# Performance work log

Hardware: AMD Instinct MI355X
Metric: run time of the kernel (lower is better)

Reference implementation:

```python
import jax, jax.numpy as jnp
import numpy as np

B, N, D, DS, LAT, FD, NF = 2, 384, 128, 3, 256, 1, 2
NPOS = DS * (2 * 5 + 1)  # 3 + 3*2*5 = 33
FREQS = np.linspace(1.0, 32.0, 5)  # torch.linspace(1, 2**5, 5)
EPS = 1e-5


def _bn(x, g, b):
    # BatchNorm1d, train-mode batch stats: normalize per channel over (batch, points)
    m = jnp.mean(x, axis=(0, 1))
    v = jnp.var(x, axis=(0, 1))
    return (x - m) * jax.lax.rsqrt(v + EPS) * g + b


def _tblock(xyz4, f, Wq, Wk, Wv, Wg1, bg1, Wg2, bg2, Wpe, bpe, g, b):
    # group_all=True full vector attention. f: [B,n,D], xyz4: [B,n,3]
    q = f @ Wq.T
    k = f @ Wk.T
    v = f @ Wv.T
    # knn_xyz gathered under no_grad in torch -> stop_gradient on the key side
    pd = xyz4[:, :, None] - jax.lax.stop_gradient(xyz4)[:, None]  # [B,n,n,3]
    parts = [pd]
    for fr in FREQS:
        parts.append(jnp.sin(pd * fr))
        parts.append(jnp.cos(pd * fr))
    pos = jnp.concatenate(parts, axis=-1) @ Wpe.T + bpe  # [B,n,n,D]
    edges = q[:, :, None] - k[:, None] + pos  # [B,n,n,D]
    h = jax.nn.relu(edges @ Wg1.T + bg1)
    attn = jax.nn.softmax(h @ Wg2.T + bg2, axis=-2)  # softmax over neighbor axis
    res = jnp.sum(attn * (v[:, None] + pos), axis=2)  # einsum bmnf,bmnf->bmf
    return _bn(res + f, g, b)


def setup_inputs() -> dict:
    key = jax.random.key(0)
    ks = iter(jax.random.split(key, 40))
    def rn(shape, s=0.05):
        return jax.random.normal(next(ks), shape, dtype=jnp.float32) * s
    z = lambda *s: jnp.zeros(s, jnp.float32)
    o = lambda *s: jnp.ones(s, jnp.float32)
    nb = NF + 1  # begin block + nfinal blocks
    return {
        "xyz": jax.random.normal(next(ks), (B, N, DS), dtype=jnp.float32),
        "feats": jax.random.normal(next(ks), (B, N, FD), dtype=jnp.float32),
        "enc_W": rn((D, FD)), "enc_b": z(D),
        "tb_Wq": rn((nb, D, D)), "tb_Wk": rn((nb, D, D)), "tb_Wv": rn((nb, D, D)),
        "tb_Wg1": rn((nb, D, D)), "tb_bg1": z(nb, D),
        "tb_Wg2": rn((nb, D, D)), "tb_bg2": z(nb, D),
        "tb_Wpe": rn((nb, D, NPOS)), "tb_bpe": z(nb, D),
        "tb_gamma": o(nb, D), "tb_beta": z(nb, D),
        "em_W1": rn((NF, D, D)), "em_b1": z(NF, D),
        "em_W2": rn((NF, D, D)), "em_b2": z(NF, D),
        "em_gamma": o(NF, D), "em_beta": z(NF, D),
        "fcf_W1": rn((LAT, D)), "fcf_b1": z(LAT),
        "fcf_W2": rn((LAT, LAT)), "fcf_b2": z(LAT),
    }


def reference(xyz, feats, enc_W, enc_b, tb_Wq, tb_Wk, tb_Wv, tb_Wg1, tb_bg1,
              tb_Wg2, tb_bg2, tb_Wpe, tb_bpe, tb_gamma, tb_beta,
              em_W1, em_b1, em_W2, em_b2, em_gamma, em_beta,
              fcf_W1, fcf_b1, fcf_W2, fcf_b2):
    f = feats @ enc_W.T + enc_b  # enc_feats
    x4 = xyz * 4.0
    for i in range(NF + 1):  # i=0: transformer_begin; i>=1: final transformers
        f = _tblock(x4, f, tb_Wq[i], tb_Wk[i], tb_Wv[i], tb_Wg1[i], tb_bg1[i],
                    tb_Wg2[i], tb_bg2[i], tb_Wpe[i], tb_bpe[i], tb_gamma[i], tb_beta[i])
        if i > 0:
            j = i - 1  # ElementwiseMLP: bn(x + relu(conv2(relu(conv1(x)))))
            y = jax.nn.relu(f @ em_W1[j].T + em_b1[j])
            y = jax.nn.relu(y @ em_W2[j].T + em_b2[j])
            f = _bn(f + y, em_gamma[j], em_beta[j])
    e = jax.nn.relu(f @ fcf_W1.T + fcf_b1) @ fcf_W2.T + fcf_b2
    return jnp.max(e, axis=1)  # lat_rep [B, lat_dim]
```

## Files before the change

### kernel.cpp

```cpp
#include <hip/hip_runtime.h>
#include <hip/hip_bf16.h>

#define B_ 2
#define N_ 384
#define D_ 128
#define LAT_ 256
#define NPOS_ 33
#define ROWS_ (B_*N_)

typedef __attribute__((ext_vector_type(8))) short bf16x8;
typedef __attribute__((ext_vector_type(4))) float f32x4;

#define MFMA(a,b,c) __builtin_amdgcn_mfma_f32_16x16x32_bf16((a),(b),(c),0,0,0)

__device__ __forceinline__ unsigned short f2bf(float x) {
    unsigned int u = __float_as_uint(x);
    u += 0x7FFFu + ((u >> 16) & 1u);
    return (unsigned short)(u >> 16);
}

__device__ __forceinline__ float bn_apply(float x, const float* stats, const float* gam,
                                          const float* bet, int d) {
    float s  = stats[d], sq = stats[128 + d];
    float mean = s * (1.f/ROWS_);
    float var  = sq * (1.f/ROWS_) - mean*mean;
    return (x - mean) * rsqrtf(var + 1e-5f) * gam[d] + bet[d];
}

__global__ __launch_bounds__(256) void enc_kernel(const float* __restrict__ feats,
                           const float* __restrict__ W,
                           const float* __restrict__ bias,
                           float* __restrict__ f) {
    int i = blockIdx.x*256 + threadIdx.x;
    if (i >= ROWS_*D_) return;
    int r = i >> 7, d = i & 127;
    f[i] = feats[r]*W[d] + bias[d];
}

__global__ __launch_bounds__(128) void qkv_kernel(const float* __restrict__ graw,
    const float* __restrict__ stats, const float* __restrict__ gam, const float* __restrict__ bet,
    int use_stats,
    const float* __restrict__ Wq, const float* __restrict__ Wk, const float* __restrict__ Wv,
    float* __restrict__ q, float* __restrict__ k, float* __restrict__ v) {
    __shared__ float row[D_];
    int r = blockIdx.x, d = threadIdx.x;
    float x = graw[r*D_+d];
    if (use_stats) x = bn_apply(x, stats, gam, bet, d);
    row[d] = x;
    __syncthreads();
    float aq=0.f, ak=0.f, av=0.f;
    #pragma unroll 4
    for (int e4=0;e4<D_/4;e4++){
        float4 wq = *(const float4*)(Wq + d*D_ + e4*4);
        float4 wk = *(const float4*)(Wk + d*D_ + e4*4);
        float4 wv = *(const float4*)(Wv + d*D_ + e4*4);
        float x0=row[e4*4+0], x1=row[e4*4+1], x2=row[e4*4+2], x3=row[e4*4+3];
        aq += wq.x*x0 + wq.y*x1 + wq.z*x2 + wq.w*x3;
        ak += wk.x*x0 + wk.y*x1 + wk.z*x2 + wk.w*x3;
        av += wv.x*x0 + wv.y*x1 + wv.z*x2 + wv.w*x3;
    }
    q[r*D_+d]=aq; k[r*D_+d]=ak; v[r*D_+d]=av;
}

__global__ __launch_bounds__(512) void attn_mfma_kernel(
    const float* __restrict__ xyz, const float* __restrict__ graw,
    const float* __restrict__ stats_in, const float* __restrict__ gam_in,
    const float* __restrict__ bet_in, int use_stats,
    const float* __restrict__ qb, const float* __restrict__ kb, const float* __restrict__ vb,
    const float* __restrict__ Wpe, const float* __restrict__ bpe,
    const float* __restrict__ Wg1, const float* __restrict__ bg1,
    const float* __restrict__ Wg2, const float* __restrict__ bg2,
    float* __restrict__ gout, float* __restrict__ stats_out)
{
    __shared__ unsigned short sParts[32*64];
    __shared__ unsigned short sX[32*128];
    __shared__ unsigned short sH[32*128];
    __shared__ float sRed[4*128];

    const int t   = threadIdx.x;
    const int w   = t >> 6;
    const int l   = t & 63;
    const int lr  = l & 15;
    const int lg  = l >> 4;
    const int rb  = w >> 2;
    const int ct0 = (w & 3) * 2;

    const int row  = blockIdx.x;
    const int b    = row / N_;
    const int brow = b * N_;

    bf16x8 bWg1[2][4], bWg2[2][4], bWpe[2][2];
    float  bpe_c[2], bg1_c[2], bg2_c[2], q_c[2];

    #pragma unroll
    for (int ct = 0; ct < 2; ++ct) {
        const int dout = (ct0 + ct) * 16 + lr;
        #pragma unroll
        for (int kt = 0; kt < 4; ++kt) {
            const float* p1 = Wg1 + dout * D_ + kt * 32 + lg * 8;
            const float* p2 = Wg2 + dout * D_ + kt * 32 + lg * 8;
            float4 a0 = *(const float4*)(p1);
            float4 a1 = *(const float4*)(p1 + 4);
            float4 c0 = *(const float4*)(p2);
            float4 c1 = *(const float4*)(p2 + 4);
            bf16x8 v1, v2;
            v1[0]=(short)f2bf(a0.x); v1[1]=(short)f2bf(a0.y); v1[2]=(short)f2bf(a0.z); v1[3]=(short)f2bf(a0.w);
            v1[4]=(short)f2bf(a1.x); v1[5]=(short)f2bf(a1.y); v1[6]=(short)f2bf(a1.z); v1[7]=(short)f2bf(a1.w);
            v2[0]=(short)f2bf(c0.x); v2[1]=(short)f2bf(c0.y); v2[2]=(short)f2bf(c0.z); v2[3]=(short)f2bf(c0.w);
            v2[4]=(short)f2bf(c1.x); v2[5]=(short)f2bf(c1.y); v2[6]=(short)f2bf(c1.z); v2[7]=(short)f2bf(c1.w);
            bWg1[ct][kt] = v1;
            bWg2[ct][kt] = v2;
        }
        #pragma unroll
        for (int kt = 0; kt < 2; ++kt) {
            bf16x8 vv;
            #pragma unroll
            for (int e = 0; e < 8; ++e) {
                const int p = kt*32 + lg*8 + e;
                const float x = (p < NPOS_) ? Wpe[dout*NPOS_ + p] : 0.f;
                vv[e] = (short)f2bf(x);
            }
            bWpe[ct][kt] = vv;
        }
        bpe_c[ct] = bpe[dout];
        bg1_c[ct] = bg1[dout];
        bg2_c[ct] = bg2[dout];
        q_c[ct]   = qb[row*D_ + dout];
    }

    const float x4m0 = 4.f*xyz[row*3+0];
    const float x4m1 = 4.f*xyz[row*3+1];
    const float x4m2 = 4.f*xyz[row*3+2];

    for (int i = t; i < 32*64/2; i += 512) ((unsigned int*)sParts)[i] = 0u;
    __syncthreads();

    auto partsgen = [&](int n0) {
        const int n = t >> 4, j = t & 15;
        const int nr = (brow + n0 + n) * 3;
        const float pd0 = x4m0 - 4.f*xyz[nr+0];
        const float pd1 = x4m1 - 4.f*xyz[nr+1];
        const float pd2 = x4m2 - 4.f*xyz[nr+2];
        auto pval = [&](int p) -> float {
            if (p < 3) return p==0?pd0:(p==1?pd1:pd2);
            const int qq = p - 3;
            const int fi = qq / 6;
            int rem = qq - fi*6;
            bool is_sin = true;
            if (rem >= 3) { rem -= 3; is_sin = false; }
            const float pdj = rem==0?pd0:(rem==1?pd1:pd2);
            const float fr = fi==0?1.f:(fi==1?8.75f:(fi==2?16.5f:(fi==3?24.25f:32.f)));
            const float a = pdj * fr;
            return is_sin ? __sinf(a) : __cosf(a);
        };
        const int sw = (n & 7) << 3;
        sParts[(n*64 + j)      ^ sw] = f2bf(pval(j));
        sParts[(n*64 + j + 16) ^ sw] = f2bf(pval(j + 16));
        if (j == 0) sParts[(n*64 + 32) ^ sw] = f2bf(pval(32));
    };

    f32x4 pos[2];
    auto posedges = [&](int n0) {
        #pragma unroll
        for (int ct = 0; ct < 2; ++ct) {
            f32x4 acc = {0.f, 0.f, 0.f, 0.f};
            #pragma unroll
            for (int kt = 0; kt < 2; ++kt) {
                const int r16 = rb*16 + lr;
                const int idx = (r16*64 + kt*32 + lg*8) ^ ((r16 & 7) << 3);
                bf16x8 a = *(const bf16x8*)&sParts[idx];
                acc = MFMA(a, bWpe[ct][kt], acc);
            }
            #pragma unroll
            for (int r = 0; r < 4; ++r) acc[r] += bpe_c[ct];
            pos[ct] = acc;
        }
        #pragma unroll
        for (int ct = 0; ct < 2; ++ct) {
            const int d = (ct0 + ct)*16 + lr;
            #pragma unroll
            for (int r = 0; r < 4; ++r) {
                const int nl = rb*16 + lg*4 + r;
                const float e = pos[ct][r] + q_c[ct] - kb[(brow + n0 + nl)*D_ + d];
                sX[(nl*128 + d) ^ ((nl & 7) << 3)] = f2bf(e);
            }
        }
    };

    partsgen(0);
    __syncthreads();
    posedges(0);
    __syncthreads();

    float res_p[2] = {0.f, 0.f}, s_p[2] = {0.f, 0.f};

    for (int it = 0; it < N_/32; ++it) {
        const int n0 = it * 32;

        f32x4 hacc[2];
        hacc[0] = (f32x4){bg1_c[0], bg1_c[0], bg1_c[0], bg1_c[0]};
        hacc[1] = (f32x4){bg1_c[1], bg1_c[1], bg1_c[1], bg1_c[1]};
        #pragma unroll
        for (int kt = 0; kt < 4; ++kt) {
            const int r16 = rb*16 + lr;
            const int idx = (r16*128 + kt*32 + lg*8) ^ ((r16 & 7) << 3);
            bf16x8 a = *(const bf16x8*)&sX[idx];
            hacc[0] = MFMA(a, bWg1[0][kt], hacc[0]);
            hacc[1] = MFMA(a, bWg1[1][kt], hacc[1]);
        }
        #pragma unroll
        for (int ct = 0; ct < 2; ++ct) {
            const int d = (ct0 + ct)*16 + lr;
            #pragma unroll
            for (int r = 0; r < 4; ++r) {
                const int nl = rb*16 + lg*4 + r;
                sH[(nl*128 + d) ^ ((nl & 7) << 3)] = f2bf(fmaxf(hacc[ct][r], 0.f));
            }
        }
        __syncthreads();

        f32x4 lacc[2];
        lacc[0] = (f32x4){bg2_c[0], bg2_c[0], bg2_c[0], bg2_c[0]};
        lacc[1] = (f32x4){bg2_c[1], bg2_c[1], bg2_c[1], bg2_c[1]};
        #pragma unroll
        for (int kt = 0; kt < 4; ++kt) {
            const int r16 = rb*16 + lr;
            const int idx = (r16*128 + kt*32 + lg*8) ^ ((r16 & 7) << 3);
            bf16x8 a = *(const bf16x8*)&sH[idx];
            lacc[0] = MFMA(a, bWg2[0][kt], lacc[0]);
            lacc[1] = MFMA(a, bWg2[1][kt], lacc[1]);
        }
        #pragma unroll
        for (int ct = 0; ct < 2; ++ct) {
            const int d = (ct0 + ct)*16 + lr;
            #pragma unroll
            for (int r = 0; r < 4; ++r) {
                const int nl = rb*16 + lg*4 + r;
                const float wgt = __expf(lacc[ct][r]);
                const float vp = vb[(brow + n0 + nl)*D_ + d] + pos[ct][r];
                res_p[ct] += wgt * vp;
                s_p[ct]   += wgt;
            }
        }
        if (it < N_/32 - 1) partsgen(n0 + 32);
        __syncthreads();

        if (it < N_/32 - 1) {
            posedges(n0 + 32);
            __syncthreads();
        }
    }

    #pragma unroll
    for (int ct = 0; ct < 2; ++ct) {
        #pragma unroll
        for (int off = 16; off < 64; off <<= 1) {
            res_p[ct] += __shfl_xor(res_p[ct], off, 64);
            s_p[ct]   += __shfl_xor(s_p[ct], off, 64);
        }
    }
    if (lg < 2) {
        const int d = (ct0 + lg)*16 + lr;
        sRed[(rb*2+0)*128 + d] = (lg == 0) ? res_p[0] : res_p[1];
        sRed[(rb*2+1)*128 + d] = (lg == 0) ? s_p[0]   : s_p[1];
    }
    __syncthreads();
    if (t < D_) {
        const float rsum = sRed[t]       + sRed[2*128 + t];
        const float ssum = sRed[128 + t] + sRed[3*128 + t];
        float fres = graw[row*D_ + t];
        if (use_stats) fres = bn_apply(fres, stats_in, gam_in, bet_in, t);
        const float val = rsum / ssum + fres;
        gout[row*D_ + t] = val;
        atomicAdd(&stats_out[t], val);
        atomicAdd(&stats_out[128 + t], val*val);
    }
}

__global__ __launch_bounds__(128) void em_kernel(const float* __restrict__ graw,
    const float* __restrict__ stats_in, const float* __restrict__ gam_in, const float* __restrict__ bet_in,
    const float* __restrict__ W1, const float* __restrict__ b1,
    const float* __restrict__ W2, const float* __restrict__ b2,
    float* __restrict__ gout, float* __restrict__ stats_out)
{
    __shared__ float row[D_], y1[D_];
    int r = blockIdx.x, d = threadIdx.x;
    float fn = bn_apply(graw[r*D_+d], stats_in, gam_in, bet_in, d);
    row[d] = fn; __syncthreads();
    float a = b1[d];
    #pragma unroll 4
    for (int e4=0;e4<D_/4;e4++){
        float4 w = *(const float4*)(W1 + d*D_ + e4*4);
        a += w.x*row[e4*4+0] + w.y*row[e4*4+1] + w.z*row[e4*4+2] + w.w*row[e4*4+3];
    }
    y1[d] = fmaxf(a,0.f); __syncthreads();
    float a2 = b2[d];
    #pragma unroll 4
    for (int e4=0;e4<D_/4;e4++){
        float4 w = *(const float4*)(W2 + d*D_ + e4*4);
        a2 += w.x*y1[e4*4+0] + w.y*y1[e4*4+1] + w.z*y1[e4*4+2] + w.w*y1[e4*4+3];
    }
    a2 = fmaxf(a2,0.f);
    const float g2 = fn + a2;
    gout[r*D_+d] = g2;
    atomicAdd(&stats_out[d], g2);
    atomicAdd(&stats_out[128+d], g2*g2);
}

__global__ __launch_bounds__(256) void final_kernel(const float* __restrict__ graw,
    const float* __restrict__ stats_in, const float* __restrict__ gam_in, const float* __restrict__ bet_in,
    const float* __restrict__ W1, const float* __restrict__ b1,
    const float* __restrict__ W2, const float* __restrict__ b2,
    float* __restrict__ e_ws)
{
    __shared__ float row[D_];
    __shared__ float h1[LAT_];
    int r = blockIdx.x, t = threadIdx.x;
    if (t < D_) row[t] = bn_apply(graw[r*D_+t], stats_in, gam_in, bet_in, t);
    __syncthreads();
    float a = b1[t];
    #pragma unroll 4
    for (int e4=0;e4<D_/4;e4++){
        float4 w = *(const float4*)(W1 + t*D_ + e4*4);
        a += w.x*row[e4*4+0] + w.y*row[e4*4+1] + w.z*row[e4*4+2] + w.w*row[e4*4+3];
    }
    h1[t] = fmaxf(a,0.f);
    __syncthreads();
    float a2 = b2[t];
    #pragma unroll 4
    for (int e4=0;e4<LAT_/4;e4++){
        float4 w = *(const float4*)(W2 + t*LAT_ + e4*4);
        a2 += w.x*h1[e4*4+0] + w.y*h1[e4*4+1] + w.z*h1[e4*4+2] + w.w*h1[e4*4+3];
    }
    e_ws[r*LAT_+t] = a2;
}

__global__ __launch_bounds__(256) void maxred_kernel(const float* __restrict__ e_ws,
                                                     float* __restrict__ out)
{
    int b = blockIdx.x, l = threadIdx.x;
    float m = -INFINITY;
    #pragma unroll 8
    for (int n=0;n<N_;n++) m = fmaxf(m, e_ws[(b*N_+n)*LAT_+l]);
    out[b*LAT_+l] = m;
}

extern "C" void kernel_launch(void* const* d_in, const int* in_sizes, int n_in,
                              void* d_out, int out_size, void* d_ws, size_t ws_size,
                              hipStream_t stream) {
    (void)in_sizes; (void)n_in; (void)out_size; (void)ws_size;
    const float* xyz    = (const float*)d_in[0];
    const float* feats  = (const float*)d_in[1];
    const float* enc_W  = (const float*)d_in[2];
    const float* enc_b  = (const float*)d_in[3];
    const float* tb_Wq  = (const float*)d_in[4];
    const float* tb_Wk  = (const float*)d_in[5];
    const float* tb_Wv  = (const float*)d_in[6];
    const float* tb_Wg1 = (const float*)d_in[7];
    const float* tb_bg1 = (const float*)d_in[8];
    const float* tb_Wg2 = (const float*)d_in[9];
    const float* tb_bg2 = (const float*)d_in[10];
    const float* tb_Wpe = (const float*)d_in[11];
    const float* tb_bpe = (const float*)d_in[12];
    const float* tb_gamma = (const float*)d_in[13];
    const float* tb_beta  = (const float*)d_in[14];
    const float* em_W1  = (const float*)d_in[15];
    const float* em_b1  = (const float*)d_in[16];
    const float* em_W2  = (const float*)d_in[17];
    const float* em_b2  = (const float*)d_in[18];
    const float* em_gamma = (const float*)d_in[19];
    const float* em_beta  = (const float*)d_in[20];
    const float* fcf_W1 = (const float*)d_in[21];
    const float* fcf_b1 = (const float*)d_in[22];
    const float* fcf_W2 = (const float*)d_in[23];
    const float* fcf_b2 = (const float*)d_in[24];
    float* out = (float*)d_out;

    float* ws   = (float*)d_ws;
    float* buf0 = ws;
    float* buf1 = buf0 + ROWS_*D_;
    float* qbuf = buf1 + ROWS_*D_;
    float* kbuf = qbuf + ROWS_*D_;
    float* vbuf = kbuf + ROWS_*D_;
    float* ebuf = vbuf + ROWS_*D_;
    float* stats = ebuf + ROWS_*LAT_;
    float* sA0 = stats;
    float* sA1 = stats + 256;
    float* sE1 = stats + 512;
    float* sA2 = stats + 768;
    float* sE2 = stats + 1024;

    hipMemsetAsync(stats, 0, 5*256*sizeof(float), stream);

    enc_kernel<<<(ROWS_*D_+255)/256, 256, 0, stream>>>(feats, enc_W, enc_b, buf0);

    const float* gz = tb_gamma;
    qkv_kernel<<<ROWS_, 128, 0, stream>>>(buf0, gz, gz, gz, 0,
                                          tb_Wq, tb_Wk, tb_Wv, qbuf, kbuf, vbuf);
    attn_mfma_kernel<<<ROWS_, 512, 0, stream>>>(xyz, buf0, gz, gz, gz, 0,
        qbuf, kbuf, vbuf,
        tb_Wpe, tb_bpe, tb_Wg1, tb_bg1, tb_Wg2, tb_bg2, buf1, sA0);
    qkv_kernel<<<ROWS_, 128, 0, stream>>>(buf1, sA0, tb_gamma, tb_beta, 1,
                                          tb_Wq + 1*D_*D_, tb_Wk + 1*D_*D_, tb_Wv + 1*D_*D_,
                                          qbuf, kbuf, vbuf);
    attn_mfma_kernel<<<ROWS_, 512, 0, stream>>>(xyz, buf1, sA0, tb_gamma, tb_beta, 1,
        qbuf, kbuf, vbuf,
        tb_Wpe + 1*D_*NPOS_, tb_bpe + 1*D_, tb_Wg1 + 1*D_*D_, tb_bg1 + 1*D_,
        tb_Wg2 + 1*D_*D_, tb_bg2 + 1*D_, buf0, sA1);
    em_kernel<<<ROWS_, 128, 0, stream>>>(buf0, sA1, tb_gamma + 1*D_, tb_beta + 1*D_,
                                         em_W1, em_b1, em_W2, em_b2, buf1, sE1);
    qkv_kernel<<<ROWS_, 128, 0, stream>>>(buf1, sE1, em_gamma, em_beta, 1,
                                          tb_Wq + 2*D_*D_, tb_Wk + 2*D_*D_, tb_Wv + 2*D_*D_,
                                          qbuf, kbuf, vbuf);
    attn_mfma_kernel<<<ROWS_, 512, 0, stream>>>(xyz, buf1, sE1, em_gamma, em_beta, 1,
        qbuf, kbuf, vbuf,
        tb_Wpe + 2*D_*NPOS_, tb_bpe + 2*D_, tb_Wg1 + 2*D_*D_, tb_bg1 + 2*D_,
        tb_Wg2 + 2*D_*D_, tb_bg2 + 2*D_, buf0, sA2);
    em_kernel<<<ROWS_, 128, 0, stream>>>(buf0, sA2, tb_gamma + 2*D_, tb_beta + 2*D_,
                                         em_W1 + 1*D_*D_, em_b1 + 1*D_,
                                         em_W2 + 1*D_*D_, em_b2 + 1*D_, buf1, sE2);
    final_kernel<<<ROWS_, 256, 0, stream>>>(buf1, sE2, em_gamma + 1*D_, em_beta + 1*D_,
                                            fcf_W1, fcf_b1, fcf_W2, fcf_b2, ebuf);
    maxred_kernel<<<B_, 256, 0, stream>>>(ebuf, out);
}
```

Before: 660.6 us.

## Process 64-neighbor tiles per iteration and prefetch K/V into registers

```diff
diff --git a/kernel.cpp b/kernel.cpp
--- a/kernel.cpp
+++ b/kernel.cpp
@@ -7,6 +7,8 @@
 #define LAT_ 256
 #define NPOS_ 33
 #define ROWS_ (B_*N_)
+#define NT_ 64
+#define ITERS_ (N_/NT_)
 
 typedef __attribute__((ext_vector_type(8))) short bf16x8;
 typedef __attribute__((ext_vector_type(4))) float f32x4;
@@ -72,9 +74,9 @@
     const float* __restrict__ Wg2, const float* __restrict__ bg2,
     float* __restrict__ gout, float* __restrict__ stats_out)
 {
-    __shared__ unsigned short sParts[32*64];
-    __shared__ unsigned short sX[32*128];
-    __shared__ unsigned short sH[32*128];
+    __shared__ unsigned short sParts[NT_*64];
+    __shared__ unsigned short sX[NT_*128];
+    __shared__ unsigned short sH[NT_*128];
     __shared__ float sRed[4*128];
 
     const int t   = threadIdx.x;
@@ -82,7 +84,7 @@
     const int l   = t & 63;
     const int lr  = l & 15;
     const int lg  = l >> 4;
-    const int rb  = w >> 2;
+    const int rb2 = w >> 2;
     const int ct0 = (w & 3) * 2;
 
     const int row  = blockIdx.x;
@@ -132,12 +134,12 @@
     const float x4m1 = 4.f*xyz[row*3+1];
     const float x4m2 = 4.f*xyz[row*3+2];
 
-    for (int i = t; i < 32*64/2; i += 512) ((unsigned int*)sParts)[i] = 0u;
+    for (int i = t; i < NT_*64/2; i += 512) ((unsigned int*)sParts)[i] = 0u;
     __syncthreads();
 
     auto partsgen = [&](int n0) {
-        const int n = t >> 4, j = t & 15;
-        const int nr = (brow + n0 + n) * 3;
+        const int rr = t >> 3, j = t & 7;
+        const int nr = (brow + n0 + rr) * 3;
         const float pd0 = x4m0 - 4.f*xyz[nr+0];
         const float pd1 = x4m1 - 4.f*xyz[nr+1];
         const float pd2 = x4m2 - 4.f*xyz[nr+2];
@@ -153,100 +155,147 @@
             const float a = pdj * fr;
             return is_sin ? __sinf(a) : __cosf(a);
         };
-        const int sw = (n & 7) << 3;
-        sParts[(n*64 + j)      ^ sw] = f2bf(pval(j));
-        sParts[(n*64 + j + 16) ^ sw] = f2bf(pval(j + 16));
-        if (j == 0) sParts[(n*64 + 32) ^ sw] = f2bf(pval(32));
+        const int sw = (rr & 7) << 3;
+        #pragma unroll
+        for (int k8 = 0; k8 < 4; ++k8) {
+            const int p = j + k8*8;
+            sParts[(rr*64 + p) ^ sw] = f2bf(pval(p));
+        }
+        if (j == 0) sParts[(rr*64 + 32) ^ sw] = f2bf(pval(32));
     };
 
-    f32x4 pos[2];
-    auto posedges = [&](int n0) {
+    float kreg[2][2][4], vreg[2][2][4];
+    auto loadK = [&](int n0) {
+        #pragma unroll
+        for (int rt = 0; rt < 2; ++rt)
+        #pragma unroll
+        for (int ct = 0; ct < 2; ++ct) {
+            const int d = (ct0 + ct)*16 + lr;
+            #pragma unroll
+            for (int r = 0; r < 4; ++r) {
+                const int rr = rb2*32 + rt*16 + lg*4 + r;
+                kreg[rt][ct][r] = kb[(brow + n0 + rr)*D_ + d];
+            }
+        }
+    };
+    auto loadV = [&](int n0) {
+        #pragma unroll
+        for (int rt = 0; rt < 2; ++rt)
+        #pragma unroll
+        for (int ct = 0; ct < 2; ++ct) {
+            const int d = (ct0 + ct)*16 + lr;
+            #pragma unroll
+            for (int r = 0; r < 4; ++r) {
+                const int rr = rb2*32 + rt*16 + lg*4 + r;
+                vreg[rt][ct][r] = vb[(brow + n0 + rr)*D_ + d];
+            }
+        }
+    };
+
+    f32x4 pos[2][2];
+    auto posedges = [&]() {
+        #pragma unroll
+        for (int rt = 0; rt < 2; ++rt)
         #pragma unroll
         for (int ct = 0; ct < 2; ++ct) {
             f32x4 acc = {0.f, 0.f, 0.f, 0.f};
             #pragma unroll
             for (int kt = 0; kt < 2; ++kt) {
-                const int r16 = rb*16 + lr;
+                const int r16 = rb2*32 + rt*16 + lr;
                 const int idx = (r16*64 + kt*32 + lg*8) ^ ((r16 & 7) << 3);
                 bf16x8 a = *(const bf16x8*)&sParts[idx];
                 acc = MFMA(a, bWpe[ct][kt], acc);
             }
             #pragma unroll
             for (int r = 0; r < 4; ++r) acc[r] += bpe_c[ct];
-            pos[ct] = acc;
-        }
+            pos[rt][ct] = acc;
+        }
+        #pragma unroll
+        for (int rt = 0; rt < 2; ++rt)
         #pragma unroll
         for (int ct = 0; ct < 2; ++ct) {
             const int d = (ct0 + ct)*16 + lr;
             #pragma unroll
             for (int r = 0; r < 4; ++r) {
-                const int nl = rb*16 + lg*4 + r;
-                const float e = pos[ct][r] + q_c[ct] - kb[(brow + n0 + nl)*D_ + d];
-                sX[(nl*128 + d) ^ ((nl & 7) << 3)] = f2bf(e);
+                const int rr = rb2*32 + rt*16 + lg*4 + r;
+                const float e = pos[rt][ct][r] + q_c[ct] - kreg[rt][ct][r];
+                sX[(rr*128 + d) ^ ((rr & 7) << 3)] = f2bf(e);
             }
         }
     };
 
     partsgen(0);
     __syncthreads();
-    posedges(0);
+    loadK(0);
+    posedges();
     __syncthreads();
 
     float res_p[2] = {0.f, 0.f}, s_p[2] = {0.f, 0.f};
 
-    for (int it = 0; it < N_/32; ++it) {
-        const int n0 = it * 32;
-
-        f32x4 hacc[2];
-        hacc[0] = (f32x4){bg1_c[0], bg1_c[0], bg1_c[0], bg1_c[0]};
-        hacc[1] = (f32x4){bg1_c[1], bg1_c[1], bg1_c[1], bg1_c[1]};
-        #pragma unroll
-        for (int kt = 0; kt < 4; ++kt) {
-            const int r16 = rb*16 + lr;
-            const int idx = (r16*128 + kt*32 + lg*8) ^ ((r16 & 7) << 3);
-            bf16x8 a = *(const bf16x8*)&sX[idx];
-            hacc[0] = MFMA(a, bWg1[0][kt], hacc[0]);
-            hacc[1] = MFMA(a, bWg1[1][kt], hacc[1]);
-        }
+    for (int it = 0; it < ITERS_; ++it) {
+        const int n0 = it * NT_;
+        const bool more = (it < ITERS_ - 1);
+
+        loadV(n0);
+        f32x4 hacc[2][2];
+        #pragma unroll
+        for (int rt = 0; rt < 2; ++rt) {
+            hacc[rt][0] = (f32x4){bg1_c[0], bg1_c[0], bg1_c[0], bg1_c[0]};
+            hacc[rt][1] = (f32x4){bg1_c[1], bg1_c[1], bg1_c[1], bg1_c[1]};
+            #pragma unroll
+            for (int kt = 0; kt < 4; ++kt) {
+                const int r16 = rb2*32 + rt*16 + lr;
+                const int idx = (r16*128 + kt*32 + lg*8) ^ ((r16 & 7) << 3);
+                bf16x8 a = *(const bf16x8*)&sX[idx];
+                hacc[rt][0] = MFMA(a, bWg1[0][kt], hacc[rt][0]);
+                hacc[rt][1] = MFMA(a, bWg1[1][kt], hacc[rt][1]);
+            }
+        }
+        #pragma unroll
+        for (int rt = 0; rt < 2; ++rt)
         #pragma unroll
         for (int ct = 0; ct < 2; ++ct) {
             const int d = (ct0 + ct)*16 + lr;
             #pragma unroll
             for (int r = 0; r < 4; ++r) {
-                const int nl = rb*16 + lg*4 + r;
-                sH[(nl*128 + d) ^ ((nl & 7) << 3)] = f2bf(fmaxf(hacc[ct][r], 0.f));
+                const int rr = rb2*32 + rt*16 + lg*4 + r;
+                sH[(rr*128 + d) ^ ((rr & 7) << 3)] = f2bf(fmaxf(hacc[rt][ct][r], 0.f));
             }
         }
         __syncthreads();
 
-        f32x4 lacc[2];
-        lacc[0] = (f32x4){bg2_c[0], bg2_c[0], bg2_c[0], bg2_c[0]};
-        lacc[1] = (f32x4){bg2_c[1], bg2_c[1], bg2_c[1], bg2_c[1]};
-        #pragma unroll
-        for (int kt = 0; kt < 4; ++kt) {
-            const int r16 = rb*16 + lr;
-            const int idx = (r16*128 + kt*32 + lg*8) ^ ((r16 & 7) << 3);
-            bf16x8 a = *(const bf16x8*)&sH[idx];
-            lacc[0] = MFMA(a, bWg2[0][kt], lacc[0]);
-            lacc[1] = MFMA(a, bWg2[1][kt], lacc[1]);
-        }
-        #pragma unroll
-        for (int ct = 0; ct < 2; ++ct) {
-            const int d = (ct0 + ct)*16 + lr;
+        if (more) loadK(n0 + NT_);
+        f32x4 lacc[2][2];
+        #pragma unroll
+        for (int rt = 0; rt < 2; ++rt) {
+            lacc[rt][0] = (f32x4){bg2_c[0], bg2_c[0], bg2_c[0], bg2_c[0]};
+            lacc[rt][1] = (f32x4){bg2_c[1], bg2_c[1], bg2_c[1], bg2_c[1]};
+            #pragma unroll
+            for (int kt = 0; kt < 4; ++kt) {
+                const int r16 = rb2*32 + rt*16 + lr;
+                const int idx = (r16*128 + kt*32 + lg*8) ^ ((r16 & 7) << 3);
+                bf16x8 a = *(const bf16x8*)&sH[idx];
+                lacc[rt][0] = MFMA(a, bWg2[0][kt], lacc[rt][0]);
+                lacc[rt][1] = MFMA(a, bWg2[1][kt], lacc[rt][1]);
+            }
+        }
+        #pragma unroll
+        for (int rt = 0; rt < 2; ++rt)
+        #pragma unroll
+        for (int ct = 0; ct < 2; ++ct) {
             #pragma unroll
             for (int r = 0; r < 4; ++r) {
-                const int nl = rb*16 + lg*4 + r;
-                const float wgt = __expf(lacc[ct][r]);
-                const float vp = vb[(brow + n0 + nl)*D_ + d] + pos[ct][r];
+                const float wgt = __expf(lacc[rt][ct][r]);
+                const float vp  = vreg[rt][ct][r] + pos[rt][ct][r];
                 res_p[ct] += wgt * vp;
                 s_p[ct]   += wgt;
             }
         }
-        if (it < N_/32 - 1) partsgen(n0 + 32);
+        if (more) partsgen(n0 + NT_);
         __syncthreads();
 
-        if (it < N_/32 - 1) {
-            posedges(n0 + 32);
+        if (more) {
+            posedges();
             __syncthreads();
         }
     }
@@ -259,10 +308,13 @@
             s_p[ct]   += __shfl_xor(s_p[ct], off, 64);
         }
     }
-    if (lg < 2) {
-        const int d = (ct0 + lg)*16 + lr;
-        sRed[(rb*2+0)*128 + d] = (lg == 0) ? res_p[0] : res_p[1];
-        sRed[(rb*2+1)*128 + d] = (lg == 0) ? s_p[0]   : s_p[1];
+    if (lg == 0) {
+        #pragma unroll
+        for (int ct = 0; ct < 2; ++ct) {
+            const int d = (ct0 + ct)*16 + lr;
+            sRed[(rb2*2+0)*128 + d] = res_p[ct];
+            sRed[(rb2*2+1)*128 + d] = s_p[ct];
+        }
     }
     __syncthreads();
     if (t < D_) {
```

Result: faster. 607.6 us (-8.0%).
